# Optimization experiments

Measured on AMD Instinct MI355X. Metric: run time of the kernel, lower is better.

The kernel has to match this reference:

```python
import jax, jax.numpy as jnp
import numpy as np

B, T = 8192, 64  # batch of independent 64x64 attention tiles

def setup_inputs() -> dict:
    key = jax.random.key(0)
    kq, kk, kv, kp, kr = jax.random.split(key, 5)
    shape = (B, T, T)
    return {
        "q": jax.random.normal(kq, shape, dtype=jnp.float32),
        "k": jax.random.normal(kk, shape, dtype=jnp.float32),
        "v": jax.random.normal(kv, shape, dtype=jnp.float32),
        "proj": jax.random.normal(kp, shape, dtype=jnp.float32),
        "residual": jax.random.normal(kr, shape, dtype=jnp.float32),
    }

def reference(q, k, v, proj, residual):
    # scores = q @ k^T on each [64,64] tile
    scores = jnp.einsum('bij,bkj->bik', q, k)
    # faithful to source: plain exp (no max-subtraction), then normalize
    scores_exp = jnp.exp(scores)
    probs = scores_exp / jnp.sum(scores_exp, axis=-1, keepdims=True)
    ctx = jnp.einsum('bij,bjk->bik', probs, v)
    proj_out = jnp.einsum('bij,bjk->bik', ctx, proj)
    return proj_out + residual
```

## Files before the change

kernel.cpp:

```cpp
#include <hip/hip_runtime.h>
#include <hip/hip_bf16.h>

typedef __attribute__((ext_vector_type(8))) short short8;
typedef __attribute__((ext_vector_type(4))) float f32x4;
typedef __attribute__((ext_vector_type(4))) unsigned short u16x4;

__device__ __forceinline__ unsigned short f2bf(float x) {
  unsigned u = __builtin_bit_cast(unsigned, x);
  u += 0x7FFFu + ((u >> 16) & 1u);
  return (unsigned short)(u >> 16);
}
__device__ __forceinline__ float bf2f(unsigned short h) {
  return __builtin_bit_cast(float, ((unsigned)h) << 16);
}

__device__ __forceinline__ int sidx(int row, int col) {
  return (row << 6) + ((((col >> 2) ^ (row & 15))) << 2) + (col & 3);
}

__device__ __forceinline__ short8 ldfrag(const unsigned short* m, int row, int kbase, int hi) {
  const int c0 = kbase + (hi << 2);
  const int rb = (row << 6);
  const int rx = row & 15;
  u16x4 a = *(const u16x4*)(m + rb + ((((c0) >> 2) ^ rx) << 2));
  u16x4 b = *(const u16x4*)(m + rb + ((((c0 + 16) >> 2) ^ rx) << 2));
  short8 f;
  f[0] = (short)a[0]; f[1] = (short)a[1]; f[2] = (short)a[2]; f[3] = (short)a[3];
  f[4] = (short)b[0]; f[5] = (short)b[1]; f[6] = (short)b[2]; f[7] = (short)b[3];
  return f;
}

__global__ __launch_bounds__(256, 3) void attn64_kernel(
    const float* __restrict__ qg, const float* __restrict__ kg,
    const float* __restrict__ vg, const float* __restrict__ pg,
    const float* __restrict__ rg, float* __restrict__ og) {
  __shared__ unsigned short sm[6 * 4096];
  unsigned short* qh = sm + 0;
  unsigned short* ql = sm + 4096;
  unsigned short* kh = sm + 8192;
  unsigned short* kl = sm + 12288;
  unsigned short* vt = sm + 16384;
  unsigned short* pt = sm + 20480;
  unsigned short* eb = sm + 0;
  unsigned short* cb = sm + 4096;

  const int tid = threadIdx.x;
  const size_t base = (size_t)blockIdx.x << 12;

  const float4* q4 = (const float4*)(qg + base);
  const float4* k4 = (const float4*)(kg + base);
  const float4* v4 = (const float4*)(vg + base);
  const float4* p4 = (const float4*)(pg + base);

  #pragma unroll
  for (int it = 0; it < 4; ++it) {
    const int i4 = tid + (it << 8);
    const int row = i4 >> 4;
    const int c4 = i4 & 15;
    const int un = (c4 ^ (row & 15)) << 2;
    {
      float4 x = q4[i4];
      unsigned short h0 = f2bf(x.x), h1 = f2bf(x.y), h2 = f2bf(x.z), h3 = f2bf(x.w);
      u16x4 hv = {h0, h1, h2, h3};
      u16x4 lv = {f2bf(x.x - bf2f(h0)), f2bf(x.y - bf2f(h1)),
                  f2bf(x.z - bf2f(h2)), f2bf(x.w - bf2f(h3))};
      *(u16x4*)(qh + (row << 6) + un) = hv;
      *(u16x4*)(ql + (row << 6) + un) = lv;
    }
    {
      float4 x = k4[i4];
      unsigned short h0 = f2bf(x.x), h1 = f2bf(x.y), h2 = f2bf(x.z), h3 = f2bf(x.w);
      u16x4 hv = {h0, h1, h2, h3};
      u16x4 lv = {f2bf(x.x - bf2f(h0)), f2bf(x.y - bf2f(h1)),
                  f2bf(x.z - bf2f(h2)), f2bf(x.w - bf2f(h3))};
      *(u16x4*)(kh + (row << 6) + un) = hv;
      *(u16x4*)(kl + (row << 6) + un) = lv;
    }
    {
      float4 x = v4[i4];
      const int r2 = c4 << 2;
      vt[sidx(r2 + 0, row)] = f2bf(x.x);
      vt[sidx(r2 + 1, row)] = f2bf(x.y);
      vt[sidx(r2 + 2, row)] = f2bf(x.z);
      vt[sidx(r2 + 3, row)] = f2bf(x.w);
    }
    {
      float4 x = p4[i4];
      const int r2 = c4 << 2;
      pt[sidx(r2 + 0, row)] = f2bf(x.x);
      pt[sidx(r2 + 1, row)] = f2bf(x.y);
      pt[sidx(r2 + 2, row)] = f2bf(x.z);
      pt[sidx(r2 + 3, row)] = f2bf(x.w);
    }
  }
  __syncthreads();

  const int l = tid & 63;
  const int w = tid >> 6;
  const int lo = l & 15;
  const int hi = l >> 4;
  const int arow = (w << 4) + lo;

  short8 aH0 = ldfrag(qh, arow, 0, hi);
  short8 aH1 = ldfrag(qh, arow, 32, hi);
  short8 aL0 = ldfrag(ql, arow, 0, hi);
  short8 aL1 = ldfrag(ql, arow, 32, hi);

  float et[4][4];
  #pragma unroll
  for (int t = 0; t < 4; ++t) {
    f32x4 acc = {0.f, 0.f, 0.f, 0.f};
    const int brow = (t << 4) + lo;
    short8 bH0 = ldfrag(kh, brow, 0, hi);
    short8 bL0 = ldfrag(kl, brow, 0, hi);
    acc = __builtin_amdgcn_mfma_f32_16x16x32_bf16(aH0, bH0, acc, 0, 0, 0);
    acc = __builtin_amdgcn_mfma_f32_16x16x32_bf16(aL0, bH0, acc, 0, 0, 0);
    acc = __builtin_amdgcn_mfma_f32_16x16x32_bf16(aH0, bL0, acc, 0, 0, 0);
    short8 bH1 = ldfrag(kh, brow, 32, hi);
    short8 bL1 = ldfrag(kl, brow, 32, hi);
    acc = __builtin_amdgcn_mfma_f32_16x16x32_bf16(aH1, bH1, acc, 0, 0, 0);
    acc = __builtin_amdgcn_mfma_f32_16x16x32_bf16(aL1, bH1, acc, 0, 0, 0);
    acc = __builtin_amdgcn_mfma_f32_16x16x32_bf16(aH1, bL1, acc, 0, 0, 0);
    #pragma unroll
    for (int j = 0; j < 4; ++j) et[t][j] = __expf(acc[j]);
  }

  float rs[4];
  #pragma unroll
  for (int j = 0; j < 4; ++j) rs[j] = (et[0][j] + et[1][j]) + (et[2][j] + et[3][j]);
  #pragma unroll
  for (int m = 1; m < 16; m <<= 1) {
    #pragma unroll
    for (int j = 0; j < 4; ++j) rs[j] += __shfl_xor(rs[j], m, 64);
  }
  float rinv[4];
  #pragma unroll
  for (int j = 0; j < 4; ++j) rinv[j] = 1.0f / rs[j];

  __syncthreads();

  #pragma unroll
  for (int t = 0; t < 4; ++t) {
    #pragma unroll
    for (int j = 0; j < 4; ++j) {
      eb[sidx((w << 4) + (hi << 2) + j, (t << 4) + lo)] = f2bf(et[t][j]);
    }
  }
  __syncthreads();

  short8 ae0 = ldfrag(eb, arow, 0, hi);
  short8 ae1 = ldfrag(eb, arow, 32, hi);
  float ctx[4][4];
  #pragma unroll
  for (int t = 0; t < 4; ++t) {
    f32x4 acc = {0.f, 0.f, 0.f, 0.f};
    const int brow = (t << 4) + lo;
    short8 b0 = ldfrag(vt, brow, 0, hi);
    short8 b1 = ldfrag(vt, brow, 32, hi);
    acc = __builtin_amdgcn_mfma_f32_16x16x32_bf16(ae0, b0, acc, 0, 0, 0);
    acc = __builtin_amdgcn_mfma_f32_16x16x32_bf16(ae1, b1, acc, 0, 0, 0);
    #pragma unroll
    for (int j = 0; j < 4; ++j) ctx[t][j] = acc[j] * rinv[j];
  }

  #pragma unroll
  for (int t = 0; t < 4; ++t) {
    #pragma unroll
    for (int j = 0; j < 4; ++j) {
      cb[sidx((w << 4) + (hi << 2) + j, (t << 4) + lo)] = f2bf(ctx[t][j]);
    }
  }
  __syncthreads();

  short8 ac0 = ldfrag(cb, arow, 0, hi);
  short8 ac1 = ldfrag(cb, arow, 32, hi);
  #pragma unroll
  for (int t = 0; t < 4; ++t) {
    f32x4 acc = {0.f, 0.f, 0.f, 0.f};
    const int brow = (t << 4) + lo;
    short8 b0 = ldfrag(pt, brow, 0, hi);
    short8 b1 = ldfrag(pt, brow, 32, hi);
    acc = __builtin_amdgcn_mfma_f32_16x16x32_bf16(ac0, b0, acc, 0, 0, 0);
    acc = __builtin_amdgcn_mfma_f32_16x16x32_bf16(ac1, b1, acc, 0, 0, 0);
    #pragma unroll
    for (int j = 0; j < 4; ++j) {
      const int off = (((w << 4) + (hi << 2) + j) << 6) + (t << 4) + lo;
      og[base + off] = acc[j] + rg[base + off];
    }
  }
}

extern "C" void kernel_launch(void* const* d_in, const int* in_sizes, int n_in,
                              void* d_out, int out_size, void* d_ws, size_t ws_size,
                              hipStream_t stream) {
  const float* q = (const float*)d_in[0];
  const float* k = (const float*)d_in[1];
  const float* v = (const float*)d_in[2];
  const float* p = (const float*)d_in[3];
  const float* r = (const float*)d_in[4];
  float* o = (float*)d_out;
  const int B = in_sizes[0] >> 12;
  attn64_kernel<<<dim3(B), dim3(256), 0, stream>>>(q, k, v, p, r, o);
}
```

Before: 153.9 us.

## Load Q fragments directly into registers, shrink LDS, retune swizzle and occupancy

Q is read straight from global memory into each lane's MFMA A-fragment registers and split into bf16 hi/lo there, so Q no longer goes through shared memory. This cuts LDS use from 48KB to 32KB per block and raises the launch-bounds occupancy hint from 3 to 5 blocks. The swizzle also XORs in bits of row>>4 to change how LDS bank conflicts fall. The direct Q loads are less coalesced (16-byte pieces per lane across rows), and the higher occupancy target may constrain registers.

Measured after the change: 152.0 us. No clear change (-1.2%).

```diff
diff --git a/kernel.cpp b/kernel.cpp
--- a/kernel.cpp
+++ b/kernel.cpp
@@ -14,59 +14,69 @@
   return __builtin_bit_cast(float, ((unsigned)h) << 16);
 }
 
+__device__ __forceinline__ int hsw(int row) { return (row & 15) ^ ((row >> 4) & 3); }
 __device__ __forceinline__ int sidx(int row, int col) {
-  return (row << 6) + ((((col >> 2) ^ (row & 15))) << 2) + (col & 3);
+  return (row << 6) + ((((col >> 2) ^ hsw(row)) & 15) << 2) + (col & 3);
 }
 
 __device__ __forceinline__ short8 ldfrag(const unsigned short* m, int row, int kbase, int hi) {
   const int c0 = kbase + (hi << 2);
-  const int rb = (row << 6);
-  const int rx = row & 15;
-  u16x4 a = *(const u16x4*)(m + rb + ((((c0) >> 2) ^ rx) << 2));
-  u16x4 b = *(const u16x4*)(m + rb + ((((c0 + 16) >> 2) ^ rx) << 2));
+  const int rb = row << 6;
+  const int hx = hsw(row);
+  u16x4 a = *(const u16x4*)(m + rb + ((((c0 >> 2) ^ hx) & 15) << 2));
+  u16x4 b = *(const u16x4*)(m + rb + (((((c0 + 16) >> 2) ^ hx) & 15) << 2));
   short8 f;
   f[0] = (short)a[0]; f[1] = (short)a[1]; f[2] = (short)a[2]; f[3] = (short)a[3];
   f[4] = (short)b[0]; f[5] = (short)b[1]; f[6] = (short)b[2]; f[7] = (short)b[3];
   return f;
 }
 
-__global__ __launch_bounds__(256, 3) void attn64_kernel(
+__device__ __forceinline__ void split4(float4 v, short8& H, short8& L, int o) {
+  unsigned short h0 = f2bf(v.x), h1 = f2bf(v.y), h2 = f2bf(v.z), h3 = f2bf(v.w);
+  H[o + 0] = (short)h0; H[o + 1] = (short)h1; H[o + 2] = (short)h2; H[o + 3] = (short)h3;
+  L[o + 0] = (short)f2bf(v.x - bf2f(h0));
+  L[o + 1] = (short)f2bf(v.y - bf2f(h1));
+  L[o + 2] = (short)f2bf(v.z - bf2f(h2));
+  L[o + 3] = (short)f2bf(v.w - bf2f(h3));
+}
+
+__global__ __launch_bounds__(256, 5) void attn64_kernel(
     const float* __restrict__ qg, const float* __restrict__ kg,
     const float* __restrict__ vg, const float* __restrict__ pg,
     const float* __restrict__ rg, float* __restrict__ og) {
-  __shared__ unsigned short sm[6 * 4096];
-  unsigned short* qh = sm + 0;
-  unsigned short* ql = sm + 4096;
-  unsigned short* kh = sm + 8192;
-  unsigned short* kl = sm + 12288;
-  unsigned short* vt = sm + 16384;
-  unsigned short* pt = sm + 20480;
+  __shared__ unsigned short sm[4 * 4096];
+  unsigned short* kh = sm + 0;
+  unsigned short* kl = sm + 4096;
+  unsigned short* vt = sm + 8192;
+  unsigned short* pt = sm + 12288;
   unsigned short* eb = sm + 0;
   unsigned short* cb = sm + 4096;
 
   const int tid = threadIdx.x;
   const size_t base = (size_t)blockIdx.x << 12;
 
-  const float4* q4 = (const float4*)(qg + base);
   const float4* k4 = (const float4*)(kg + base);
   const float4* v4 = (const float4*)(vg + base);
   const float4* p4 = (const float4*)(pg + base);
+
+  const int l = tid & 63;
+  const int w = tid >> 6;
+  const int lo = l & 15;
+  const int hi = l >> 4;
+  const int arow = (w << 4) + lo;
+
+  const float* qrow = qg + base + ((size_t)arow << 6);
+  float4 xq0 = *(const float4*)(qrow + (hi << 2));
+  float4 xq1 = *(const float4*)(qrow + 16 + (hi << 2));
+  float4 xq2 = *(const float4*)(qrow + 32 + (hi << 2));
+  float4 xq3 = *(const float4*)(qrow + 48 + (hi << 2));
 
   #pragma unroll
   for (int it = 0; it < 4; ++it) {
     const int i4 = tid + (it << 8);
     const int row = i4 >> 4;
     const int c4 = i4 & 15;
-    const int un = (c4 ^ (row & 15)) << 2;
-    {
-      float4 x = q4[i4];
-      unsigned short h0 = f2bf(x.x), h1 = f2bf(x.y), h2 = f2bf(x.z), h3 = f2bf(x.w);
-      u16x4 hv = {h0, h1, h2, h3};
-      u16x4 lv = {f2bf(x.x - bf2f(h0)), f2bf(x.y - bf2f(h1)),
-                  f2bf(x.z - bf2f(h2)), f2bf(x.w - bf2f(h3))};
-      *(u16x4*)(qh + (row << 6) + un) = hv;
-      *(u16x4*)(ql + (row << 6) + un) = lv;
-    }
+    const int un = ((c4 ^ hsw(row)) & 15) << 2;
     {
       float4 x = k4[i4];
       unsigned short h0 = f2bf(x.x), h1 = f2bf(x.y), h2 = f2bf(x.z), h3 = f2bf(x.w);
@@ -93,18 +103,14 @@
       pt[sidx(r2 + 3, row)] = f2bf(x.w);
     }
   }
-  __syncthreads();
-
-  const int l = tid & 63;
-  const int w = tid >> 6;
-  const int lo = l & 15;
-  const int hi = l >> 4;
-  const int arow = (w << 4) + lo;
-
-  short8 aH0 = ldfrag(qh, arow, 0, hi);
-  short8 aH1 = ldfrag(qh, arow, 32, hi);
-  short8 aL0 = ldfrag(ql, arow, 0, hi);
-  short8 aL1 = ldfrag(ql, arow, 32, hi);
+
+  short8 aH0, aL0, aH1, aL1;
+  split4(xq0, aH0, aL0, 0);
+  split4(xq1, aH0, aL0, 4);
+  split4(xq2, aH1, aL1, 0);
+  split4(xq3, aH1, aL1, 4);
+
+  __syncthreads();
 
   float et[4][4];
   #pragma unroll
```
